# Performance work log

Measured on AMD Instinct MI355X. Metric: run time of the kernel, lower is better.

## Reference

```python
import jax, jax.numpy as jnp
import numpy as np

THRESH = 0.3
LENS = 0.5

@jax.custom_vjp
def spike_fn(x):
    return (x > 0).astype(x.dtype)

def _spike_fwd(x):
    return spike_fn(x), x

def _spike_bwd(x, g):
    # boxcar surrogate gradient: 1/(2*lens) for |x| < lens
    return (g * (jnp.abs(x) < LENS).astype(g.dtype) / (2.0 * LENS),)

spike_fn.defvjp(_spike_fwd, _spike_bwd)


def setup_inputs() -> dict:
    key = jax.random.key(0)
    ks = jax.random.split(key, 9)
    B, T, N_in, H, O = 256, 64, 700, 2048, 20
    s_ih = 1.0 / np.sqrt(N_in)
    s_hh = 1.0 / np.sqrt(H)
    s_ho = 1.0 / np.sqrt(H)
    return {
        "input": jax.random.uniform(ks[0], (B, T, N_in), dtype=jnp.float32),
        "W_ih": jax.random.normal(ks[1], (H, N_in), dtype=jnp.float32) * s_ih,
        "b_ih": jax.random.normal(ks[2], (H,), dtype=jnp.float32) * s_ih,
        "W_hh": jax.random.normal(ks[3], (H, H), dtype=jnp.float32) * s_hh,
        "b_hh": jax.random.normal(ks[4], (H,), dtype=jnp.float32) * s_hh,
        "W_ho": jax.random.normal(ks[5], (O, H), dtype=jnp.float32) * s_ho,
        "b_ho": jax.random.normal(ks[6], (O,), dtype=jnp.float32) * s_ho,
        "tau_m_h": jnp.full((1,), 20.0, dtype=jnp.float32),
        "tau_m_o": jnp.full((1,), 20.0, dtype=jnp.float32),
    }


def reference(input, W_ih, b_ih, W_hh, b_hh, W_ho, b_ho, tau_m_h, tau_m_o):
    B, T, _ = input.shape
    H = W_ih.shape[0]
    O = W_ho.shape[0]
    alpha_h = jnp.exp(-1.0 / tau_m_h)  # [1], broadcasts over [B, H]
    alpha_o = jnp.exp(-1.0 / tau_m_o)

    # Precompute input projection for all steps: [T, B, H]
    x_proj = jnp.einsum("bti,hi->tbh", input, W_ih) + b_ih

    def step(carry, xp):
        h_mem, h_spike, o_mem, o_spike, o_sum = carry
        # recurrent LIF hidden update
        h_mem = h_mem * alpha_h * (1.0 - h_spike) + xp + h_spike @ W_hh.T + b_hh
        h_spike = spike_fn(h_mem - THRESH)
        # output LIF update
        o_mem = o_mem * alpha_o * (1.0 - o_spike) + h_spike @ W_ho.T + b_ho
        o_spike = spike_fn(o_mem - THRESH)
        o_sum = o_sum + o_spike
        return (h_mem, h_spike, o_mem, o_spike, o_sum), None

    zH = jnp.zeros((B, H), dtype=input.dtype)
    zO = jnp.zeros((B, O), dtype=input.dtype)
    (_, _, _, _, o_sumspike), _ = jax.lax.scan(step, (zH, zH, zO, zO, zO), x_proj)
    return o_sumspike / T
```

## Files before the change

kernel.cpp:

```cpp
#include <hip/hip_runtime.h>
#include <stdint.h>

typedef __attribute__((ext_vector_type(4))) int i32x4;

static constexpr int BB = 256, TT = 64, NIN = 700, NKP = 768, HH = 2048, OO = 20;
static constexpr float THRESH_V = 0.3f;
static constexpr int NBLK = 256;
static constexpr int NREC = 16;
static constexpr int XNIT = 11;
static constexpr int NIT  = NREC + XNIT;

static constexpr size_t OFF_HMEM  = 0;
static constexpr size_t OFF_SPK0  = 2097152;
static constexpr size_t OFF_OMEM  = 2621440;
static constexpr size_t OFF_OSPK  = 2641920;
static constexpr size_t OFF_OSUM  = 2662400;
static constexpr size_t ZERO_END  = 2682880;
static constexpr size_t OFF_SPK1  = 2682880;
static constexpr size_t OFF_ALPHA = 3207168;
static constexpr size_t OFF_WHHD  = 3207424;
static constexpr size_t WHH_PLANE = 4194304;
static constexpr size_t OFF_WIHD  = 19984640;
static constexpr size_t WIH_PLANE = 1572864;
static constexpr size_t OFF_XD    = 26276096;
static constexpr size_t XD_PLANE  = 12582912;
static constexpr size_t WS_NEED   = 76607744;

#define WAIT_VM6()  asm volatile("s_waitcnt vmcnt(6)" ::: "memory")
#define WAIT_VM3()  asm volatile("s_waitcnt vmcnt(3)" ::: "memory")
#define WAIT_VM0()  asm volatile("s_waitcnt vmcnt(0)" ::: "memory")
#define SCHED0()    __builtin_amdgcn_sched_barrier(0)

__device__ __forceinline__ void wdig(float w, double scale, signed char d[4]) {
    int q = (int)rint((double)w * scale);
    int t0 = (int)(signed char)(q & 0xFF); q = (q - t0) >> 8;
    int t1 = (int)(signed char)(q & 0xFF); q = (q - t1) >> 8;
    int t2 = (int)(signed char)(q & 0xFF); q = (q - t2) >> 8;
    d[0] = (signed char)t0; d[1] = (signed char)t1;
    d[2] = (signed char)t2; d[3] = (signed char)q;
}

__device__ __forceinline__ i32x4 ld_rec(const uint8_t* base, int row, int sl) {
    return *reinterpret_cast<const i32x4*>(base + row * 128 + ((sl ^ (row & 7)) << 4));
}
__device__ __forceinline__ i32x4 ld_x(const uint8_t* base, int row, int s) {
    int phys = (s + (row >> 1)) & 3;
    return *reinterpret_cast<const i32x4*>(base + row * 64 + (phys << 4));
}

__device__ __forceinline__ void gload(const uint8_t* src, uint8_t* dst) {
    __builtin_amdgcn_global_load_lds((const __attribute__((address_space(1))) void*)src,
                                     (__attribute__((address_space(3))) void*)dst, 16, 0, 0);
}

__device__ __forceinline__ void stage_rec(uint8_t* buf, const int8_t* spk, const int8_t* whhd,
                                          int m0, int n0, int k0B, int wid, int lane) {
#pragma unroll
    for (int i = 0; i < 3; ++i) {
        int u = wid * 3 + i;
        if (u < 8) {
            int row = u * 8 + (lane >> 3);
            int s   = (lane & 7) ^ (row & 7);
            gload((const uint8_t*)spk + (size_t)(m0 + row) * HH + k0B + (s << 4),
                  buf + u * 1024);
        } else {
            int v = u - 8, p = v >> 2, sub = v & 3;
            int row = sub * 8 + (lane >> 3);
            int s   = (lane & 7) ^ (row & 7);
            gload((const uint8_t*)whhd + (size_t)p * WHH_PLANE +
                  (size_t)(n0 + row) * HH + k0B + (s << 4),
                  buf + 8192 + p * 4096 + sub * 1024);
        }
    }
}
__device__ __forceinline__ void stage_x(uint8_t* buf, const int8_t* xd_t, const int8_t* wihd,
                                        int m0, int n0, int k0B, int wid, int lane) {
#pragma unroll
    for (int i = 0; i < 3; ++i) {
        int u = wid * 3 + i;
        if (u < 16) {
            int p = u >> 2, sub = u & 3;
            int row = sub * 16 + (lane >> 2);
            int s   = ((lane & 3) - (row >> 1)) & 3;
            gload((const uint8_t*)xd_t + (size_t)p * XD_PLANE +
                  (size_t)(m0 + row) * NKP + k0B + (s << 4),
                  buf + p * 4096 + sub * 1024);
        } else {
            int v = u - 16, p = v >> 1, sub = v & 1;
            int row = sub * 16 + (lane >> 2);
            int s   = ((lane & 3) - (row >> 1)) & 3;
            gload((const uint8_t*)wihd + (size_t)p * WIH_PLANE +
                  (size_t)(n0 + row) * NKP + k0B + (s << 4),
                  buf + 16384 + p * 2048 + sub * 1024);
        }
    }
}

__device__ __forceinline__ void mfma_rec(const uint8_t* buf, int mw, int nw, int fr, int hi4,
                                         i32x4 aR[4]) {
#pragma unroll
    for (int ks = 0; ks < 2; ++ks) {
        int sl = ks * 4 + hi4;
        i32x4 a = ld_rec(buf, mw * 16 + fr, sl);
#pragma unroll
        for (int p = 0; p < 4; ++p) {
            i32x4 b = ld_rec(buf + 8192 + p * 4096, nw * 16 + fr, sl);
            aR[p] = __builtin_amdgcn_mfma_i32_16x16x64_i8(a, b, aR[p], 0, 0, 0);
        }
    }
}
__device__ __forceinline__ void mfma_x(const uint8_t* buf, int mw, int nw, int fr, int hi4,
                                       i32x4 aX[5]) {
    i32x4 fa[4], fb[4];
#pragma unroll
    for (int p = 0; p < 4; ++p) {
        fa[p] = ld_x(buf + p * 4096,         mw * 16 + fr, hi4);
        fb[p] = ld_x(buf + 16384 + p * 2048, nw * 16 + fr, hi4);
    }
#pragma unroll
    for (int a = 0; a < 4; ++a)
#pragma unroll
        for (int b = 0; b < 4; ++b) {
            if (a + b < 2) continue;
            const int c = a + b - 2;
            aX[c] = __builtin_amdgcn_mfma_i32_16x16x64_i8(fa[a], fb[b], aX[c], 0, 0, 0);
        }
}

__global__ __launch_bounds__(256) void conv_whh_i8(const float* __restrict__ W,
                                                   int8_t* __restrict__ p0, int8_t* __restrict__ p1,
                                                   int8_t* __restrict__ p2, int8_t* __restrict__ p3,
                                                   const float* __restrict__ tau_h,
                                                   const float* __restrict__ tau_o,
                                                   float* __restrict__ alpha) {
    int idx = blockIdx.x * 256 + threadIdx.x;
    if (idx == 0) {
        float qh = __fdiv_rn(-1.0f, tau_h[0]);
        float qo = __fdiv_rn(-1.0f, tau_o[0]);
        alpha[0] = (float)exp((double)qh);
        alpha[1] = (float)exp((double)qo);
    }
    float4 v = reinterpret_cast<const float4*>(W)[idx];
    signed char dx[4], dy[4], dz[4], dw[4];
    const double SC = 1073741824.0;
    wdig(v.x, SC, dx); wdig(v.y, SC, dy); wdig(v.z, SC, dz); wdig(v.w, SC, dw);
    reinterpret_cast<char4*>(p0)[idx] = make_char4(dx[0], dy[0], dz[0], dw[0]);
    reinterpret_cast<char4*>(p1)[idx] = make_char4(dx[1], dy[1], dz[1], dw[1]);
    reinterpret_cast<char4*>(p2)[idx] = make_char4(dx[2], dy[2], dz[2], dw[2]);
    reinterpret_cast<char4*>(p3)[idx] = make_char4(dx[3], dy[3], dz[3], dw[3]);
}

__global__ __launch_bounds__(256) void conv_wih_i8(const float* __restrict__ W,
                                                   int8_t* __restrict__ p0, int8_t* __restrict__ p1,
                                                   int8_t* __restrict__ p2, int8_t* __restrict__ p3) {
    int row = blockIdx.x;
    for (int i = threadIdx.x; i < NKP; i += 256) {
        float v = (i < NIN) ? W[(size_t)row * NIN + i] : 0.f;
        signed char d[4];
        wdig(v, 1073741824.0, d);
        size_t o = (size_t)row * NKP + i;
        p0[o] = d[0]; p1[o] = d[1]; p2[o] = d[2]; p3[o] = d[3];
    }
}

__global__ __launch_bounds__(256) void conv_x_i8(const float* __restrict__ in,
                                                 int8_t* __restrict__ p0, int8_t* __restrict__ p1,
                                                 int8_t* __restrict__ p2, int8_t* __restrict__ p3) {
    int blk = blockIdx.x;
    int t = blk >> 8, b = blk & 255;
    const float* src = in + ((size_t)b * TT + t) * NIN;
    size_t dst = ((size_t)t * BB + b) * NKP;
    for (int i = threadIdx.x; i < NKP; i += 256) {
        float v = (i < NIN) ? src[i] : 0.f;
        signed char d[4];
        wdig(v, 16777216.0, d);
        p0[dst + i] = d[0]; p1[dst + i] = d[1]; p2[dst + i] = d[2]; p3[dst + i] = d[3];
    }
}

__device__ __forceinline__ void odot_block(int g, int wid, int lane, const int8_t* __restrict__ spk,
                                           const float* __restrict__ W_ho,
                                           const float* __restrict__ b_ho,
                                           float a_o, float* __restrict__ o_mem,
                                           float* __restrict__ o_spk, float* __restrict__ o_sum,
                                           float* __restrict__ out ) {
    const int8_t* srow = spk + (size_t)g * HH + lane * 32;
    int4 s0 = *reinterpret_cast<const int4*>(srow);
    int4 s1 = *reinterpret_cast<const int4*>(srow + 16);
    int sw[8] = {s0.x, s0.y, s0.z, s0.w, s1.x, s1.y, s1.z, s1.w};
#pragma unroll 1
    for (int p = 0; p < 3; ++p) {
        int o = wid + 8 * p;
        if (o >= OO) break;
        const float* wrow = W_ho + (size_t)o * HH + lane * 32;
        double acc = 0.0;
#pragma unroll
        for (int q = 0; q < 8; ++q) {
            float4 w = *reinterpret_cast<const float4*>(wrow + q * 4);
            int sv = sw[q];
            acc += (sv & 0x000000FF) ? (double)w.x : 0.0;
            acc += (sv & 0x0000FF00) ? (double)w.y : 0.0;
            acc += (sv & 0x00FF0000) ? (double)w.z : 0.0;
            acc += (sv & 0xFF000000) ? (double)w.w : 0.0;
        }
#pragma unroll
        for (int off = 32; off >= 1; off >>= 1)
            acc += __shfl_xor(acc, off, 64);
        if (lane == 0) {
            float dot = (float)acc;
            size_t oo = (size_t)g * OO + o;
            float om = o_mem[oo], osp = o_spk[oo];
            float v = __fadd_rn(__fadd_rn(__fmul_rn(__fmul_rn(om, a_o), 1.f - osp), dot), b_ho[o]);
            float sn = (v > THRESH_V) ? 1.f : 0.f;
            o_mem[oo] = v;
            o_spk[oo] = sn;
            float s = __fadd_rn(o_sum[oo], sn);
            o_sum[oo] = s;
            if (out) out[oo] = __fmul_rn(s, 1.f / 64.f);
        }
    }
}

__global__ __launch_bounds__(512) void step_kernel(
    const int8_t* __restrict__ whhd, const int8_t* __restrict__ wihd,
    const int8_t* __restrict__ xd,
    const int8_t* __restrict__ spk_rd, int8_t* __restrict__ spk_wr,
    float* __restrict__ h_mem, const float* __restrict__ alpha,
    const float* __restrict__ b_ih, const float* __restrict__ b_hh,
    const float* __restrict__ W_ho, const float* __restrict__ b_ho,
    float* __restrict__ o_mem, float* __restrict__ o_spk, float* __restrict__ o_sum,
    int t) {
    __shared__ __align__(16) uint8_t L0[24576];
    __shared__ __align__(16) uint8_t L1[24576];
    __shared__ __align__(16) uint8_t L2[24576];
    __shared__ __align__(16) uint8_t L3[24576];

    int g   = blockIdx.x;
    int tid = threadIdx.x;
    int lane = tid & 63, wid = tid >> 6;
    int m0 = (g >> 6) * 64;
    int n0 = (g & 63) * 32;
    int mw = wid >> 1, nw = wid & 1;
    int fr = lane & 15, hi4 = lane >> 4;

    const int8_t* xd_t = xd + (size_t)t * BB * NKP;

    i32x4 aR[4] = {};
    i32x4 aX[5] = {};

    stage_rec(L0, spk_rd, whhd, m0, n0, 0,   wid, lane);
    stage_rec(L1, spk_rd, whhd, m0, n0, 128, wid, lane);
    stage_rec(L2, spk_rd, whhd, m0, n0, 256, wid, lane);

#pragma unroll
    for (int h = 0; h < NIT; ++h) {
        if (h < NIT - 2) { WAIT_VM6(); }
        else if (h == NIT - 2) { WAIT_VM3(); }
        else { WAIT_VM0(); }
        SCHED0();
        __builtin_amdgcn_s_barrier();
        if (h + 3 < NIT) {
            uint8_t* nb = ((h + 3) & 3) == 0 ? L0 : ((h + 3) & 3) == 1 ? L1
                        : ((h + 3) & 3) == 2 ? L2 : L3;
            int c = h + 3;
            if (c < NREC) stage_rec(nb, spk_rd, whhd, m0, n0, c * 128, wid, lane);
            else          stage_x(nb, xd_t, wihd, m0, n0, (c - NREC) * 64, wid, lane);
        }
        const uint8_t* cb = (h & 3) == 0 ? L0 : (h & 3) == 1 ? L1
                          : (h & 3) == 2 ? L2 : L3;
        __builtin_amdgcn_s_setprio(1);
        if (h < NREC) mfma_rec(cb, mw, nw, fr, hi4, aR);
        else          mfma_x(cb, mw, nw, fr, hi4, aX);
        __builtin_amdgcn_s_setprio(0);
    }

    float a_h = alpha[0];
    int j  = n0 + nw * 16 + fr;
    int rq = hi4 * 4;
#pragma unroll
    for (int rr = 0; rr < 4; ++rr) {
        int b = m0 + mw * 16 + rq + rr;
        size_t off = (size_t)b * HH + j;
        float recf = (float)((double)aR[3][rr] * 0x1p-6
                           + (double)aR[2][rr] * 0x1p-14
                           + (double)aR[1][rr] * 0x1p-22
                           + (double)aR[0][rr] * 0x1p-30);
        double xp64 = (double)aX[4][rr] * 0x1p-6
                    + (double)aX[3][rr] * 0x1p-14
                    + (double)aX[2][rr] * 0x1p-22
                    + (double)aX[1][rr] * 0x1p-30
                    + (double)aX[0][rr] * 0x1p-38;
        float xpf = (float)xp64;
        float xpb = __fadd_rn(xpf, b_ih[j]);
        float hv  = h_mem[off];
        float keep = spk_rd[off] ? 0.f : 1.f;
        float v = __fadd_rn(__fmul_rn(__fmul_rn(hv, a_h), keep), xpb);
        v = __fadd_rn(v, recf);
        v = __fadd_rn(v, b_hh[j]);
        h_mem[off] = v;
        spk_wr[off] = (v > THRESH_V) ? (int8_t)1 : (int8_t)0;
    }

    if (t > 0)
        odot_block(g, wid, lane, spk_rd, W_ho, b_ho, alpha[1], o_mem, o_spk, o_sum, nullptr);
}

__global__ __launch_bounds__(512) void final_kernel(const int8_t* __restrict__ spk,
                                                    const float* __restrict__ W_ho,
                                                    const float* __restrict__ b_ho,
                                                    const float* __restrict__ alpha,
                                                    float* __restrict__ o_mem,
                                                    float* __restrict__ o_spk,
                                                    float* __restrict__ o_sum,
                                                    float* __restrict__ out) {
    int lane = threadIdx.x & 63, wid = threadIdx.x >> 6;
    odot_block(blockIdx.x, wid, lane, spk, W_ho, b_ho, alpha[1], o_mem, o_spk, o_sum, out);
}

extern "C" void kernel_launch(void* const* d_in, const int* in_sizes, int n_in,
                              void* d_out, int out_size, void* d_ws, size_t ws_size,
                              hipStream_t stream) {
    const float* in    = (const float*)d_in[0];
    const float* W_ih  = (const float*)d_in[1];
    const float* b_ih  = (const float*)d_in[2];
    const float* W_hh  = (const float*)d_in[3];
    const float* b_hh  = (const float*)d_in[4];
    const float* W_ho  = (const float*)d_in[5];
    const float* b_ho  = (const float*)d_in[6];
    const float* tau_h = (const float*)d_in[7];
    const float* tau_o = (const float*)d_in[8];

    uint8_t* ws = (uint8_t*)d_ws;
    float*  h_mem = (float*)(ws + OFF_HMEM);
    int8_t* spk0  = (int8_t*)(ws + OFF_SPK0);
    float*  o_mem = (float*)(ws + OFF_OMEM);
    float*  o_spk = (float*)(ws + OFF_OSPK);
    float*  o_sum = (float*)(ws + OFF_OSUM);
    int8_t* spk1  = (int8_t*)(ws + OFF_SPK1);
    float*  alpha = (float*)(ws + OFF_ALPHA);
    int8_t* whhd  = (int8_t*)(ws + OFF_WHHD);
    int8_t* wihd  = (int8_t*)(ws + OFF_WIHD);
    int8_t* xd    = (int8_t*)(ws + OFF_XD);

    if (ws_size < WS_NEED) return;

    hipMemsetAsync(ws, 0, ZERO_END, stream);
    conv_whh_i8<<<4096, 256, 0, stream>>>(W_hh,
                                          whhd, whhd + WHH_PLANE, whhd + 2 * WHH_PLANE, whhd + 3 * WHH_PLANE,
                                          tau_h, tau_o, alpha);
    conv_wih_i8<<<2048, 256, 0, stream>>>(W_ih,
                                          wihd, wihd + WIH_PLANE, wihd + 2 * WIH_PLANE, wihd + 3 * WIH_PLANE);
    conv_x_i8<<<16384, 256, 0, stream>>>(in,
                                         xd, xd + XD_PLANE, xd + 2 * XD_PLANE, xd + 3 * XD_PLANE);

    for (int t = 0; t < TT; ++t) {
        const int8_t* srd = (t & 1) ? spk1 : spk0;
        int8_t*       swr = (t & 1) ? spk0 : spk1;
        step_kernel<<<NBLK, 512, 0, stream>>>(whhd, wihd, xd, srd, swr, h_mem, alpha,
                                              b_ih, b_hh, W_ho, b_ho,
                                              o_mem, o_spk, o_sum, t);
    }
    final_kernel<<<NBLK, 512, 0, stream>>>(spk0, W_ho, b_ho, alpha, o_mem, o_spk, o_sum,
                                           (float*)d_out);
}
```

Baseline: 1.243 ms.

## Stage two K-chunks per barrier and remap output dot work across blocks

The recurrent step kernel's single-chunk, depth-3 pipeline becomes a two-chunk-per-phase schedule with a full vmcnt(0) wait. Each barrier now covers two staged chunks and two MFMA chunks, which halves the number of barriers. To keep the chunk count even, the input-projection loop grows from 11 to 12 chunks, so the padded K region is now processed too. The output-layer dot product is also redistributed: each wave picks a (batch, output) pair from a flat index instead of one block owning one batch row. In exchange, the full memory wait removes part of the load/compute overlap, and the extra chunk adds some work.

```diff
diff --git a/kernel.cpp b/kernel.cpp
--- a/kernel.cpp
+++ b/kernel.cpp
@@ -7,8 +7,9 @@
 static constexpr float THRESH_V = 0.3f;
 static constexpr int NBLK = 256;
 static constexpr int NREC = 16;
-static constexpr int XNIT = 11;
+static constexpr int XNIT = 12;
 static constexpr int NIT  = NREC + XNIT;
+static constexpr int NPH  = NIT / 2;
 
 static constexpr size_t OFF_HMEM  = 0;
 static constexpr size_t OFF_SPK0  = 2097152;
@@ -26,8 +27,6 @@
 static constexpr size_t XD_PLANE  = 12582912;
 static constexpr size_t WS_NEED   = 76607744;
 
-#define WAIT_VM6()  asm volatile("s_waitcnt vmcnt(6)" ::: "memory")
-#define WAIT_VM3()  asm volatile("s_waitcnt vmcnt(3)" ::: "memory")
 #define WAIT_VM0()  asm volatile("s_waitcnt vmcnt(0)" ::: "memory")
 #define SCHED0()    __builtin_amdgcn_sched_barrier(0)
 
@@ -184,15 +183,18 @@
                                            float a_o, float* __restrict__ o_mem,
                                            float* __restrict__ o_spk, float* __restrict__ o_sum,
                                            float* __restrict__ out ) {
-    const int8_t* srow = spk + (size_t)g * HH + lane * 32;
-    int4 s0 = *reinterpret_cast<const int4*>(srow);
-    int4 s1 = *reinterpret_cast<const int4*>(srow + 16);
-    int sw[8] = {s0.x, s0.y, s0.z, s0.w, s1.x, s1.y, s1.z, s1.w};
 #pragma unroll 1
-    for (int p = 0; p < 3; ++p) {
-        int o = wid + 8 * p;
-        if (o >= OO) break;
-        const float* wrow = W_ho + (size_t)o * HH + lane * 32;
+    for (int k = 0; k < 3; ++k) {
+        int j = wid + 8 * k;
+        if (j >= 20) break;
+        int pair = g * 20 + j;
+        int b = pair & 255;
+        int o = pair >> 8;
+        const int8_t* srow = spk  + (size_t)b * HH + lane * 32;
+        const float*  wrow = W_ho + (size_t)o * HH + lane * 32;
+        int4 s0 = *reinterpret_cast<const int4*>(srow);
+        int4 s1 = *reinterpret_cast<const int4*>(srow + 16);
+        int sw[8] = {s0.x, s0.y, s0.z, s0.w, s1.x, s1.y, s1.z, s1.w};
         double acc = 0.0;
 #pragma unroll
         for (int q = 0; q < 8; ++q) {
@@ -208,7 +210,7 @@
             acc += __shfl_xor(acc, off, 64);
         if (lane == 0) {
             float dot = (float)acc;
-            size_t oo = (size_t)g * OO + o;
+            size_t oo = (size_t)b * OO + o;
             float om = o_mem[oo], osp = o_spk[oo];
             float v = __fadd_rn(__fadd_rn(__fmul_rn(__fmul_rn(om, a_o), 1.f - osp), dot), b_ho[o]);
             float sn = (v > THRESH_V) ? 1.f : 0.f;
@@ -248,29 +250,33 @@
     i32x4 aR[4] = {};
     i32x4 aX[5] = {};
 
-    stage_rec(L0, spk_rd, whhd, m0, n0, 0,   wid, lane);
-    stage_rec(L1, spk_rd, whhd, m0, n0, 128, wid, lane);
-    stage_rec(L2, spk_rd, whhd, m0, n0, 256, wid, lane);
-
-#pragma unroll
-    for (int h = 0; h < NIT; ++h) {
-        if (h < NIT - 2) { WAIT_VM6(); }
-        else if (h == NIT - 2) { WAIT_VM3(); }
-        else { WAIT_VM0(); }
+    auto BUF = [&](int c) -> uint8_t* {
+        return (c & 3) == 0 ? L0 : (c & 3) == 1 ? L1 : (c & 3) == 2 ? L2 : L3;
+    };
+    auto STAGE = [&](int c) {
+        if (c < NREC) stage_rec(BUF(c), spk_rd, whhd, m0, n0, c * 128, wid, lane);
+        else          stage_x(BUF(c), xd_t, wihd, m0, n0, (c - NREC) * 64, wid, lane);
+    };
+    auto MFMA = [&](int c) {
+        if (c < NREC) mfma_rec(BUF(c), mw, nw, fr, hi4, aR);
+        else          mfma_x(BUF(c), mw, nw, fr, hi4, aX);
+    };
+
+    STAGE(0);
+    STAGE(1);
+
+#pragma unroll
+    for (int ph = 0; ph < NPH; ++ph) {
+        WAIT_VM0();
         SCHED0();
         __builtin_amdgcn_s_barrier();
-        if (h + 3 < NIT) {
-            uint8_t* nb = ((h + 3) & 3) == 0 ? L0 : ((h + 3) & 3) == 1 ? L1
-                        : ((h + 3) & 3) == 2 ? L2 : L3;
-            int c = h + 3;
-            if (c < NREC) stage_rec(nb, spk_rd, whhd, m0, n0, c * 128, wid, lane);
-            else          stage_x(nb, xd_t, wihd, m0, n0, (c - NREC) * 64, wid, lane);
-        }
-        const uint8_t* cb = (h & 3) == 0 ? L0 : (h & 3) == 1 ? L1
-                          : (h & 3) == 2 ? L2 : L3;
+        if (ph + 1 < NPH) {
+            STAGE(2 * ph + 2);
+            STAGE(2 * ph + 3);
+        }
         __builtin_amdgcn_s_setprio(1);
-        if (h < NREC) mfma_rec(cb, mw, nw, fr, hi4, aR);
-        else          mfma_x(cb, mw, nw, fr, hi4, aX);
+        MFMA(2 * ph);
+        MFMA(2 * ph + 1);
         __builtin_amdgcn_s_setprio(0);
     }
 
```

Result: slower. 1.413 ms (+13.7%).
